# Kernel optimization log

Hardware: AMD Instinct MI355X
Metric: run time of the kernel (lower is better)

## Reference

```python
import jax, jax.numpy as jnp
import numpy as np

B, S, P, J = 32, 128, 2, 17
DIN, DOUT, DRNN, DHID = 2, 3, 128, 256
N = P * J
DT = 0.1   # delta_t from init
K = 4      # Euler steps, hardcoded k=int(4) in source


def setup_inputs() -> dict:
    key = jax.random.key(0)
    ks = jax.random.split(key, 12)
    g = lambda k, sh, fan: (jax.random.normal(k, sh, jnp.float32) / np.sqrt(fan)).astype(jnp.float32)
    d = {}
    d['x2d'] = jax.random.normal(ks[0], (B, S, P, J, DIN), jnp.float32)
    d['mask'] = jax.random.randint(ks[1], (B, S, P, J, 1), 0, 2).astype(jnp.int32)
    # ODE MLP: DRNN -> DHID -> DHID -> DRNN (num_hidden=2 hidden layers, tanh)
    d['ode_w0'] = g(ks[2], (DRNN, DHID), DRNN); d['ode_b0'] = jnp.zeros((DHID,), jnp.float32)
    d['ode_w1'] = g(ks[3], (DHID, DHID), DHID); d['ode_b1'] = jnp.zeros((DHID,), jnp.float32)
    d['ode_w2'] = g(ks[4], (DHID, DRNN), DHID); d['ode_b2'] = jnp.zeros((DRNN,), jnp.float32)
    # GRU cell 0: input DIN -> hidden DRNN ; GRU cell 1: input DRNN -> hidden DRNN
    d['wih0'] = g(ks[5], (DIN, 3 * DRNN), DIN);  d['whh0'] = g(ks[6], (DRNN, 3 * DRNN), DRNN)
    d['bih0'] = jnp.zeros((3 * DRNN,), jnp.float32); d['bhh0'] = jnp.zeros((3 * DRNN,), jnp.float32)
    d['wih1'] = g(ks[7], (DRNN, 3 * DRNN), DRNN); d['whh1'] = g(ks[8], (DRNN, 3 * DRNN), DRNN)
    d['bih1'] = jnp.zeros((3 * DRNN,), jnp.float32); d['bhh1'] = jnp.zeros((3 * DRNN,), jnp.float32)
    d['wout'] = g(ks[9], (DRNN, DOUT), DRNN); d['bout'] = jnp.zeros((DOUT,), jnp.float32)
    d['h0'] = 0.01 * jax.random.normal(ks[10], (1, 1, DRNN), jnp.float32)
    return d


def _ode(h, w0, b0, w1, b1, w2, b2):
    h = jnp.tanh(h @ w0 + b0)
    h = jnp.tanh(h @ w1 + b1)
    return h @ w2 + b2


def _gru(x, h, wih, whh, bih, bhh):
    gi = x @ wih + bih
    gh = h @ whh + bhh
    ir, iz, ig = jnp.split(gi, 3, axis=-1)
    hr, hz, hg = jnp.split(gh, 3, axis=-1)
    r = jax.nn.sigmoid(ir + hr)
    z = jax.nn.sigmoid(iz + hz)
    n = jnp.tanh(ig + r * hg)
    return (1.0 - z) * n + z * h


def reference(x2d, mask, ode_w0, ode_b0, ode_w1, ode_b1, ode_w2, ode_b2,
              wih0, whh0, bih0, bhh0, wih1, whh1, bih1, bhh1, wout, bout, h0):
    m = mask.astype(x2d.dtype)                      # (B,S,P,J,1)
    xs = (x2d * m).reshape(B, S, N, DIN)            # masked 2D input
    ms = m.reshape(B, S, N, 1)
    h_init = jnp.broadcast_to(h0, (B, N, DRNN))

    def step(h, inp):
        x, mm = inp                                 # (B,N,DIN), (B,N,1)
        h1 = h
        for _ in range(K):                          # 4 Euler ODE steps
            h1 = h1 + DT * _ode(h1, ode_w0, ode_b0, ode_w1, ode_b1, ode_w2, ode_b2)
        h2 = _gru(x, h1, wih0, whh0, bih0, bhh0)    # stacked GRU, both conditioned on h1
        h2 = _gru(h2, h1, wih1, whh1, bih1, bhh1)
        h_next = h1 * (1.0 - mm) + h2 * mm
        return h_next, h1

    _, hs = jax.lax.scan(step, h_init,
                         (jnp.swapaxes(xs, 0, 1), jnp.swapaxes(ms, 0, 1)))
    hs = jnp.swapaxes(hs, 0, 1)                     # (B,S,N,DRNN)
    ys = (hs @ wout + bout).reshape(B, S, P, J, DOUT)
    return ys
```

## Files before the change

kernel.cpp:

```cpp
#include <hip/hip_runtime.h>

typedef _Float16 f16x8 __attribute__((ext_vector_type(8)));
typedef float f32x4 __attribute__((ext_vector_type(4)));

constexpr int S_ = 128;
constexpr float DT_ = 0.1f;
constexpr float LS = 2048.0f;
constexpr float INV = 1.0f / 2048.0f;

#define MFMA(a, b, c) __builtin_amdgcn_mfma_f32_16x16x32_f16((a), (b), (c), 0, 0, 0)

#define OB0   0
#define OB1   256
#define OB2   512
#define OBHH0 640
#define OBIH0 1024
#define OBIH1 1408
#define OBHH1 1792
#define NBIAS 2176

__device__ __forceinline__ float fast_tanh(float x) {
    float e = __expf(2.0f * x);
    return 1.0f - 2.0f / (e + 1.0f);
}
__device__ __forceinline__ float fast_sigmoid(float x) {
    return 1.0f / (1.0f + __expf(-x));
}

template<int KT>
__device__ __forceinline__ void wtile_mm(
    const float* __restrict__ W, int N, int nt,
    const _Float16* __restrict__ Ah, const _Float16* __restrict__ Al, int lda,
    int lrow, int lk8, f32x4& acc, f32x4& pe, f32x4& qe)
{
    const float* base = W + (size_t)lk8 * N + nt * 16 + lrow;
    float raw[KT][8];
#pragma unroll
    for (int kt = 0; kt < KT; ++kt)
#pragma unroll
        for (int j = 0; j < 8; ++j)
            raw[kt][j] = base[(kt * 32 + j) * (size_t)N];
#pragma unroll
    for (int kt = 0; kt < KT; ++kt) {
        f16x8 bh, bl;
#pragma unroll
        for (int j = 0; j < 8; ++j) {
            float v = raw[kt][j];
            _Float16 h = (_Float16)v;
            bh[j] = h;
            bl[j] = (_Float16)((v - (float)h) * LS);
        }
        f16x8 ah = *(const f16x8*)(Ah + lrow * lda + kt * 32 + lk8);
        f16x8 al = *(const f16x8*)(Al + lrow * lda + kt * 32 + lk8);
        acc = MFMA(ah, bh, acc);
        pe  = MFMA(ah, bl, pe);
        qe  = MFMA(al, bh, qe);
    }
}

__global__ __launch_bounds__(512, 2) void odernn_mfma(
    const float* __restrict__ x2d, const int* __restrict__ maskp,
    const float* __restrict__ w0, const float* __restrict__ b0,
    const float* __restrict__ w1, const float* __restrict__ b1,
    const float* __restrict__ w2, const float* __restrict__ b2,
    const float* __restrict__ wih0, const float* __restrict__ whh0,
    const float* __restrict__ bih0, const float* __restrict__ bhh0,
    const float* __restrict__ wih1, const float* __restrict__ whh1,
    const float* __restrict__ bih1, const float* __restrict__ bhh1,
    const float* __restrict__ wout, const float* __restrict__ bout,
    const float* __restrict__ h0, float* __restrict__ out)
{
    __shared__ float hF[16][128];
    __shared__ _Float16 bAh[16][264], bAl[16][264];
    __shared__ _Float16 bBh[16][264], bBl[16][264];
    __shared__ _Float16 bHh[16][136], bHl[16][136];
    __shared__ float sbias[NBIAS];
    __shared__ float swi0[768];
    __shared__ float swout[384];
    __shared__ float sbout[4];
    __shared__ float sx0[16], sx1[16], smm[16];
    __shared__ int sIdx[16];

    const int tid = (int)threadIdx.x;
    const int wv = tid >> 6;
    const int l = tid & 63;
    const int lrow = l & 15;
    const int lk8 = (l >> 4) << 3;
    const int rbase = (l >> 4) << 2;

    for (int e = tid; e < 256; e += 512) { sbias[OB0 + e] = b0[e]; sbias[OB1 + e] = b1[e]; }
    for (int e = tid; e < 128; e += 512) sbias[OB2 + e] = b2[e];
    for (int e = tid; e < 384; e += 512) {
        sbias[OBHH0 + e] = bhh0[e];
        sbias[OBIH0 + e] = bih0[e];
        sbias[OBIH1 + e] = bih1[e];
        sbias[OBHH1 + e] = bhh1[e];
        swout[e] = wout[e];
    }
    for (int e = tid; e < 768; e += 512) swi0[e] = wih0[e];
    if (tid < 3) sbout[tid] = bout[tid];
    for (int e = tid; e < 2048; e += 512) {
        int row = e >> 7, col = e & 127;
        float v = h0[col];
        hF[row][col] = v;
        _Float16 hh = (_Float16)v;
        bHh[row][col] = hh;
        bHl[row][col] = (_Float16)((v - (float)hh) * LS);
    }
    if (tid < 16) {
        int grow = (int)blockIdx.x * 16 + tid;
        int bb = grow / 34, nn = grow - bb * 34;
        sIdx[tid] = bb * (S_ * 34) + nn;
    }
    __syncthreads();

    for (int s = 0; s < S_; ++s) {
        if (tid < 16) {
            int idx = sIdx[tid] + s * 34;
            float fm = (float)maskp[idx];
            smm[tid] = fm;
            sx0[tid] = x2d[2 * idx] * fm;
            sx1[tid] = x2d[2 * idx + 1] * fm;
        }

        for (int it = 0; it < 4; ++it) {
            {
                const int n0 = wv << 4, n1 = (wv + 8) << 4;
                float bv0 = sbias[OB0 + n0 + lrow], bv1 = sbias[OB0 + n1 + lrow];
                f32x4 a0 = {bv0, bv0, bv0, bv0}, a1 = {bv1, bv1, bv1, bv1};
                f32x4 p0 = {0, 0, 0, 0}, q0 = {0, 0, 0, 0}, p1 = {0, 0, 0, 0}, q1 = {0, 0, 0, 0};
                wtile_mm<4>(w0, 256, wv,     &bHh[0][0], &bHl[0][0], 136, lrow, lk8, a0, p0, q0);
                wtile_mm<4>(w0, 256, wv + 8, &bHh[0][0], &bHl[0][0], 136, lrow, lk8, a1, p1, q1);
#pragma unroll
                for (int r = 0; r < 4; ++r) {
                    int row = rbase + r;
                    float v0 = fast_tanh(a0[r] + (p0[r] + q0[r]) * INV);
                    float v1 = fast_tanh(a1[r] + (p1[r] + q1[r]) * INV);
                    _Float16 hh = (_Float16)v0;
                    bBh[row][n0 + lrow] = hh;
                    bBl[row][n0 + lrow] = (_Float16)((v0 - (float)hh) * LS);
                    hh = (_Float16)v1;
                    bBh[row][n1 + lrow] = hh;
                    bBl[row][n1 + lrow] = (_Float16)((v1 - (float)hh) * LS);
                }
            }
            __syncthreads();

            {
                const int n0 = wv << 4, n1 = (wv + 8) << 4;
                float bv0 = sbias[OB1 + n0 + lrow], bv1 = sbias[OB1 + n1 + lrow];
                f32x4 a0 = {bv0, bv0, bv0, bv0}, a1 = {bv1, bv1, bv1, bv1};
                f32x4 p0 = {0, 0, 0, 0}, q0 = {0, 0, 0, 0}, p1 = {0, 0, 0, 0}, q1 = {0, 0, 0, 0};
                wtile_mm<8>(w1, 256, wv,     &bBh[0][0], &bBl[0][0], 264, lrow, lk8, a0, p0, q0);
                wtile_mm<8>(w1, 256, wv + 8, &bBh[0][0], &bBl[0][0], 264, lrow, lk8, a1, p1, q1);
#pragma unroll
                for (int r = 0; r < 4; ++r) {
                    int row = rbase + r;
                    float v0 = fast_tanh(a0[r] + (p0[r] + q0[r]) * INV);
                    float v1 = fast_tanh(a1[r] + (p1[r] + q1[r]) * INV);
                    _Float16 hh = (_Float16)v0;
                    bAh[row][n0 + lrow] = hh;
                    bAl[row][n0 + lrow] = (_Float16)((v0 - (float)hh) * LS);
                    hh = (_Float16)v1;
                    bAh[row][n1 + lrow] = hh;
                    bAl[row][n1 + lrow] = (_Float16)((v1 - (float)hh) * LS);
                }
            }
            __syncthreads();

            {
                const int n0 = wv << 4;
                float bv = sbias[OB2 + n0 + lrow];
                f32x4 acc = {bv, bv, bv, bv};
                f32x4 pp = {0, 0, 0, 0}, qq = {0, 0, 0, 0};
                wtile_mm<8>(w2, 128, wv, &bAh[0][0], &bAl[0][0], 264, lrow, lk8, acc, pp, qq);
#pragma unroll
                for (int r = 0; r < 4; ++r) {
                    int row = rbase + r, col = n0 + lrow;
                    float v = hF[row][col] + DT_ * (acc[r] + (pp[r] + qq[r]) * INV);
                    hF[row][col] = v;
                    _Float16 hh = (_Float16)v;
                    bHh[row][col] = hh;
                    bHl[row][col] = (_Float16)((v - (float)hh) * LS);
                }
            }
            __syncthreads();
        }

        {
            f32x4 acc0, acc1, acc2;
            f32x4 p0 = {0,0,0,0}, q0 = {0,0,0,0}, p1 = {0,0,0,0}, q1 = {0,0,0,0}, p2 = {0,0,0,0}, q2 = {0,0,0,0};
            {
                float v0 = sbias[OBHH0 + ((wv) << 4) + lrow];
                float v1 = sbias[OBHH0 + ((wv + 8) << 4) + lrow];
                float v2 = sbias[OBHH0 + ((wv + 16) << 4) + lrow];
                acc0 = (f32x4){v0, v0, v0, v0};
                acc1 = (f32x4){v1, v1, v1, v1};
                acc2 = (f32x4){v2, v2, v2, v2};
            }
            wtile_mm<4>(whh0, 384, wv,      &bHh[0][0], &bHl[0][0], 136, lrow, lk8, acc0, p0, q0);
            wtile_mm<4>(whh0, 384, wv + 8,  &bHh[0][0], &bHl[0][0], 136, lrow, lk8, acc1, p1, q1);
            wtile_mm<4>(whh0, 384, wv + 16, &bHh[0][0], &bHl[0][0], 136, lrow, lk8, acc2, p2, q2);
            {
                int yrow = wv + ((l >> 5) << 3);
                int ll = l & 31;
                int c0 = ll << 2;
                float4 hv = *(const float4*)&hF[yrow][c0];
                float y0 = hv.x * swout[c0 * 3] + hv.y * swout[(c0 + 1) * 3] +
                           hv.z * swout[(c0 + 2) * 3] + hv.w * swout[(c0 + 3) * 3];
                float y1 = hv.x * swout[c0 * 3 + 1] + hv.y * swout[(c0 + 1) * 3 + 1] +
                           hv.z * swout[(c0 + 2) * 3 + 1] + hv.w * swout[(c0 + 3) * 3 + 1];
                float y2 = hv.x * swout[c0 * 3 + 2] + hv.y * swout[(c0 + 1) * 3 + 2] +
                           hv.z * swout[(c0 + 2) * 3 + 2] + hv.w * swout[(c0 + 3) * 3 + 2];
#pragma unroll
                for (int m = 16; m >= 1; m >>= 1) {
                    y0 += __shfl_xor(y0, m, 64);
                    y1 += __shfl_xor(y1, m, 64);
                    y2 += __shfl_xor(y2, m, 64);
                }
                if (ll == 0) {
                    int idx = sIdx[yrow] + s * 34;
                    out[idx * 3 + 0] = y0 + sbout[0];
                    out[idx * 3 + 1] = y1 + sbout[1];
                    out[idx * 3 + 2] = y2 + sbout[2];
                }
            }
            {
                int col = (wv << 4) + lrow;
                float wxr0 = swi0[col], wxr1 = swi0[384 + col];
                float wxz0 = swi0[128 + col], wxz1 = swi0[384 + 128 + col];
                float wxn0 = swi0[256 + col], wxn1 = swi0[384 + 256 + col];
                float bir = sbias[OBIH0 + col], biz = sbias[OBIH0 + 128 + col], bin = sbias[OBIH0 + 256 + col];
#pragma unroll
                for (int r = 0; r < 4; ++r) {
                    int row = rbase + r;
                    float ghr = acc0[r] + (p0[r] + q0[r]) * INV;
                    float ghz = acc1[r] + (p1[r] + q1[r]) * INV;
                    float ghn = acc2[r] + (p2[r] + q2[r]) * INV;
                    float xa = sx0[row], xb = sx1[row];
                    float rg = fast_sigmoid(bir + xa * wxr0 + xb * wxr1 + ghr);
                    float zg = fast_sigmoid(biz + xa * wxz0 + xb * wxz1 + ghz);
                    float nn = fast_tanh(bin + xa * wxn0 + xb * wxn1 + rg * ghn);
                    float h1 = hF[row][col];
                    float h2 = (1.0f - zg) * nn + zg * h1;
                    _Float16 hh = (_Float16)h2;
                    bBh[row][col] = hh;
                    bBl[row][col] = (_Float16)((h2 - (float)hh) * LS);
                }
            }
        }
        __syncthreads();

        {
            f32x4 gi0, gi1, gi2;
            {
                f32x4 a0, a1, a2;
                f32x4 p0 = {0,0,0,0}, q0 = {0,0,0,0}, p1 = {0,0,0,0}, q1 = {0,0,0,0}, p2 = {0,0,0,0}, q2 = {0,0,0,0};
                {
                    float v0 = sbias[OBIH1 + ((wv) << 4) + lrow];
                    float v1 = sbias[OBIH1 + ((wv + 8) << 4) + lrow];
                    float v2 = sbias[OBIH1 + ((wv + 16) << 4) + lrow];
                    a0 = (f32x4){v0, v0, v0, v0};
                    a1 = (f32x4){v1, v1, v1, v1};
                    a2 = (f32x4){v2, v2, v2, v2};
                }
                wtile_mm<4>(wih1, 384, wv,      &bBh[0][0], &bBl[0][0], 264, lrow, lk8, a0, p0, q0);
                wtile_mm<4>(wih1, 384, wv + 8,  &bBh[0][0], &bBl[0][0], 264, lrow, lk8, a1, p1, q1);
                wtile_mm<4>(wih1, 384, wv + 16, &bBh[0][0], &bBl[0][0], 264, lrow, lk8, a2, p2, q2);
                gi0 = a0 + (p0 + q0) * INV;
                gi1 = a1 + (p1 + q1) * INV;
                gi2 = a2 + (p2 + q2) * INV;
            }

            f32x4 aH0, aH1, aH2;
            f32x4 pH0 = {0,0,0,0}, qH0 = {0,0,0,0}, pH1 = {0,0,0,0}, qH1 = {0,0,0,0}, pH2 = {0,0,0,0}, qH2 = {0,0,0,0};
            {
                float v0 = sbias[OBHH1 + ((wv) << 4) + lrow];
                float v1 = sbias[OBHH1 + ((wv + 8) << 4) + lrow];
                float v2 = sbias[OBHH1 + ((wv + 16) << 4) + lrow];
                aH0 = (f32x4){v0, v0, v0, v0};
                aH1 = (f32x4){v1, v1, v1, v1};
                aH2 = (f32x4){v2, v2, v2, v2};
            }
            wtile_mm<4>(whh1, 384, wv,      &bHh[0][0], &bHl[0][0], 136, lrow, lk8, aH0, pH0, qH0);
            wtile_mm<4>(whh1, 384, wv + 8,  &bHh[0][0], &bHl[0][0], 136, lrow, lk8, aH1, pH1, qH1);
            wtile_mm<4>(whh1, 384, wv + 16, &bHh[0][0], &bHl[0][0], 136, lrow, lk8, aH2, pH2, qH2);

            __syncthreads();
#pragma unroll
            for (int r = 0; r < 4; ++r) {
                int row = rbase + r, col = (wv << 4) + lrow;
                float ghr = aH0[r] + (pH0[r] + qH0[r]) * INV;
                float ghz = aH1[r] + (pH1[r] + qH1[r]) * INV;
                float ghn = aH2[r] + (pH2[r] + qH2[r]) * INV;
                float rg = fast_sigmoid(gi0[r] + ghr);
                float zg = fast_sigmoid(gi1[r] + ghz);
                float nn = fast_tanh(gi2[r] + rg * ghn);
                float h1 = hF[row][col];
                float h2 = (1.0f - zg) * nn + zg * h1;
                float v = (smm[row] != 0.0f) ? h2 : h1;
                hF[row][col] = v;
                _Float16 hh = (_Float16)v;
                bHh[row][col] = hh;
                bHl[row][col] = (_Float16)((v - (float)hh) * LS);
            }
        }
        __syncthreads();
    }
}

extern "C" void kernel_launch(void* const* d_in, const int* in_sizes, int n_in,
                              void* d_out, int out_size, void* d_ws, size_t ws_size,
                              hipStream_t stream) {
    const float* x2d  = (const float*)d_in[0];
    const int*   mask = (const int*)d_in[1];
    const float* w0   = (const float*)d_in[2];
    const float* b0   = (const float*)d_in[3];
    const float* w1   = (const float*)d_in[4];
    const float* b1   = (const float*)d_in[5];
    const float* w2   = (const float*)d_in[6];
    const float* b2   = (const float*)d_in[7];
    const float* wih0 = (const float*)d_in[8];
    const float* whh0 = (const float*)d_in[9];
    const float* bih0 = (const float*)d_in[10];
    const float* bhh0 = (const float*)d_in[11];
    const float* wih1 = (const float*)d_in[12];
    const float* whh1 = (const float*)d_in[13];
    const float* bih1 = (const float*)d_in[14];
    const float* bhh1 = (const float*)d_in[15];
    const float* wout = (const float*)d_in[16];
    const float* bout = (const float*)d_in[17];
    const float* h0   = (const float*)d_in[18];
    float* out = (float*)d_out;

    hipLaunchKernelGGL(odernn_mfma, dim3(68), dim3(512), 0, stream,
        x2d, mask, w0, b0, w1, b1, w2, b2,
        wih0, whh0, bih0, bhh0, wih1, whh1, bih1, bhh1,
        wout, bout, h0, out);
}
```

Before: 7.217 ms.

## Pre-split weights into fp16 hi/lo tiles in MFMA fragment layout

Adds a prep kernel that converts each fp32 weight matrix once per call into fp16 high and scaled-low parts, stored in the exact per-lane MFMA B-fragment order in workspace. The main recurrent kernel then loads two contiguous 16-byte vectors per k-tile instead of eight strided fp32 loads plus conversion on every timestep. This removes repeated strided global gathers and conversion ALU work from the sequential loop. In exchange it adds six small prep launches and doubles weight storage in fp16 form. Launch bounds change from two blocks per CU to one, which relaxes register limits for the held fragments.

```diff
diff --git a/kernel.cpp b/kernel.cpp
--- a/kernel.cpp
+++ b/kernel.cpp
@@ -26,46 +26,61 @@
 __device__ __forceinline__ float fast_sigmoid(float x) {
     return 1.0f / (1.0f + __expf(-x));
 }
+__device__ __forceinline__ f32x4 bc4(float v) { return (f32x4){v, v, v, v}; }
+
+__global__ void prep_hl(const float* __restrict__ src, _Float16* __restrict__ hi,
+                        _Float16* __restrict__ lo, int K, int N) {
+    int e = blockIdx.x * 256 + threadIdx.x;
+    if (e >= K * N) return;
+    int tile = e >> 9, r = e & 511;
+    int lane = r >> 3, j = r & 7;
+    int KT = K >> 5;
+    int nt = tile / KT, kt = tile - nt * KT;
+    int k = kt * 32 + ((lane >> 4) << 3) + j;
+    int n = nt * 16 + (lane & 15);
+    float v = src[k * N + n];
+    _Float16 h = (_Float16)v;
+    hi[e] = h;
+    lo[e] = (_Float16)((v - (float)h) * LS);
+}
 
 template<int KT>
-__device__ __forceinline__ void wtile_mm(
-    const float* __restrict__ W, int N, int nt,
+__device__ __forceinline__ f32x4 tile_mm(
+    const _Float16* __restrict__ Wh, const _Float16* __restrict__ Wl, int nt,
     const _Float16* __restrict__ Ah, const _Float16* __restrict__ Al, int lda,
-    int lrow, int lk8, f32x4& acc, f32x4& pe, f32x4& qe)
+    int l, int lrow, int lk8, float bias)
 {
-    const float* base = W + (size_t)lk8 * N + nt * 16 + lrow;
-    float raw[KT][8];
-#pragma unroll
-    for (int kt = 0; kt < KT; ++kt)
-#pragma unroll
-        for (int j = 0; j < 8; ++j)
-            raw[kt][j] = base[(kt * 32 + j) * (size_t)N];
+    const _Float16* ph = Wh + ((size_t)nt * KT) * 512 + l * 8;
+    const _Float16* pl = Wl + ((size_t)nt * KT) * 512 + l * 8;
+    f16x8 bh[KT], bl[KT];
 #pragma unroll
     for (int kt = 0; kt < KT; ++kt) {
-        f16x8 bh, bl;
-#pragma unroll
-        for (int j = 0; j < 8; ++j) {
-            float v = raw[kt][j];
-            _Float16 h = (_Float16)v;
-            bh[j] = h;
-            bl[j] = (_Float16)((v - (float)h) * LS);
-        }
+        bh[kt] = *(const f16x8*)(ph + kt * 512);
+        bl[kt] = *(const f16x8*)(pl + kt * 512);
+    }
+    f32x4 acc = bc4(bias), pe = bc4(0.f), qe = bc4(0.f);
+#pragma unroll
+    for (int kt = 0; kt < KT; ++kt) {
         f16x8 ah = *(const f16x8*)(Ah + lrow * lda + kt * 32 + lk8);
         f16x8 al = *(const f16x8*)(Al + lrow * lda + kt * 32 + lk8);
-        acc = MFMA(ah, bh, acc);
-        pe  = MFMA(ah, bl, pe);
-        qe  = MFMA(al, bh, qe);
-    }
-}
-
-__global__ __launch_bounds__(512, 2) void odernn_mfma(
+        acc = MFMA(ah, bh[kt], acc);
+        pe  = MFMA(ah, bl[kt], pe);
+        qe  = MFMA(al, bh[kt], qe);
+    }
+    return acc + (pe + qe) * INV;
+}
+
+__global__ __launch_bounds__(512, 1) void odernn_mfma(
     const float* __restrict__ x2d, const int* __restrict__ maskp,
-    const float* __restrict__ w0, const float* __restrict__ b0,
-    const float* __restrict__ w1, const float* __restrict__ b1,
-    const float* __restrict__ w2, const float* __restrict__ b2,
-    const float* __restrict__ wih0, const float* __restrict__ whh0,
-    const float* __restrict__ bih0, const float* __restrict__ bhh0,
-    const float* __restrict__ wih1, const float* __restrict__ whh1,
+    const _Float16* __restrict__ w0h, const _Float16* __restrict__ w0l,
+    const _Float16* __restrict__ w1hg, const _Float16* __restrict__ w1lg,
+    const _Float16* __restrict__ w2h, const _Float16* __restrict__ w2l,
+    const _Float16* __restrict__ hh0h, const _Float16* __restrict__ hh0l,
+    const _Float16* __restrict__ ih1h, const _Float16* __restrict__ ih1l,
+    const _Float16* __restrict__ hh1h, const _Float16* __restrict__ hh1l,
+    const float* __restrict__ b0, const float* __restrict__ b1,
+    const float* __restrict__ b2, const float* __restrict__ bhh0,
+    const float* __restrict__ bih0, const float* __restrict__ wih0,
     const float* __restrict__ bih1, const float* __restrict__ bhh1,
     const float* __restrict__ wout, const float* __restrict__ bout,
     const float* __restrict__ h0, float* __restrict__ out)
@@ -125,59 +140,54 @@
 
         for (int it = 0; it < 4; ++it) {
             {
+                f32x4 v0 = tile_mm<4>(w0h, w0l, wv, &bHh[0][0], &bHl[0][0], 136,
+                                      l, lrow, lk8, sbias[OB0 + (wv << 4) + lrow]);
+                f32x4 v1 = tile_mm<4>(w0h, w0l, wv + 8, &bHh[0][0], &bHl[0][0], 136,
+                                      l, lrow, lk8, sbias[OB0 + ((wv + 8) << 4) + lrow]);
                 const int n0 = wv << 4, n1 = (wv + 8) << 4;
-                float bv0 = sbias[OB0 + n0 + lrow], bv1 = sbias[OB0 + n1 + lrow];
-                f32x4 a0 = {bv0, bv0, bv0, bv0}, a1 = {bv1, bv1, bv1, bv1};
-                f32x4 p0 = {0, 0, 0, 0}, q0 = {0, 0, 0, 0}, p1 = {0, 0, 0, 0}, q1 = {0, 0, 0, 0};
-                wtile_mm<4>(w0, 256, wv,     &bHh[0][0], &bHl[0][0], 136, lrow, lk8, a0, p0, q0);
-                wtile_mm<4>(w0, 256, wv + 8, &bHh[0][0], &bHl[0][0], 136, lrow, lk8, a1, p1, q1);
 #pragma unroll
                 for (int r = 0; r < 4; ++r) {
                     int row = rbase + r;
-                    float v0 = fast_tanh(a0[r] + (p0[r] + q0[r]) * INV);
-                    float v1 = fast_tanh(a1[r] + (p1[r] + q1[r]) * INV);
-                    _Float16 hh = (_Float16)v0;
+                    float t0 = fast_tanh(v0[r]);
+                    float t1 = fast_tanh(v1[r]);
+                    _Float16 hh = (_Float16)t0;
                     bBh[row][n0 + lrow] = hh;
-                    bBl[row][n0 + lrow] = (_Float16)((v0 - (float)hh) * LS);
-                    hh = (_Float16)v1;
+                    bBl[row][n0 + lrow] = (_Float16)((t0 - (float)hh) * LS);
+                    hh = (_Float16)t1;
                     bBh[row][n1 + lrow] = hh;
-                    bBl[row][n1 + lrow] = (_Float16)((v1 - (float)hh) * LS);
+                    bBl[row][n1 + lrow] = (_Float16)((t1 - (float)hh) * LS);
                 }
             }
             __syncthreads();
 
             {
+                f32x4 v0 = tile_mm<8>(w1hg, w1lg, wv, &bBh[0][0], &bBl[0][0], 264,
+                                      l, lrow, lk8, sbias[OB1 + (wv << 4) + lrow]);
+                f32x4 v1 = tile_mm<8>(w1hg, w1lg, wv + 8, &bBh[0][0], &bBl[0][0], 264,
+                                      l, lrow, lk8, sbias[OB1 + ((wv + 8) << 4) + lrow]);
                 const int n0 = wv << 4, n1 = (wv + 8) << 4;
-                float bv0 = sbias[OB1 + n0 + lrow], bv1 = sbias[OB1 + n1 + lrow];
-                f32x4 a0 = {bv0, bv0, bv0, bv0}, a1 = {bv1, bv1, bv1, bv1};
-                f32x4 p0 = {0, 0, 0, 0}, q0 = {0, 0, 0, 0}, p1 = {0, 0, 0, 0}, q1 = {0, 0, 0, 0};
-                wtile_mm<8>(w1, 256, wv,     &bBh[0][0], &bBl[0][0], 264, lrow, lk8, a0, p0, q0);
-                wtile_mm<8>(w1, 256, wv + 8, &bBh[0][0], &bBl[0][0], 264, lrow, lk8, a1, p1, q1);
 #pragma unroll
                 for (int r = 0; r < 4; ++r) {
                     int row = rbase + r;
-                    float v0 = fast_tanh(a0[r] + (p0[r] + q0[r]) * INV);
-                    float v1 = fast_tanh(a1[r] + (p1[r] + q1[r]) * INV);
-                    _Float16 hh = (_Float16)v0;
+                    float t0 = fast_tanh(v0[r]);
+                    float t1 = fast_tanh(v1[r]);
+                    _Float16 hh = (_Float16)t0;
                     bAh[row][n0 + lrow] = hh;
-                    bAl[row][n0 + lrow] = (_Float16)((v0 - (float)hh) * LS);
-                    hh = (_Float16)v1;
+                    bAl[row][n0 + lrow] = (_Float16)((t0 - (float)hh) * LS);
+                    hh = (_Float16)t1;
                     bAh[row][n1 + lrow] = hh;
-                    bAl[row][n1 + lrow] = (_Float16)((v1 - (float)hh) * LS);
+                    bAl[row][n1 + lrow] = (_Float16)((t1 - (float)hh) * LS);
                 }
             }
             __syncthreads();
 
             {
-                const int n0 = wv << 4;
-                float bv = sbias[OB2 + n0 + lrow];
-                f32x4 acc = {bv, bv, bv, bv};
-                f32x4 pp = {0, 0, 0, 0}, qq = {0, 0, 0, 0};
-                wtile_mm<8>(w2, 128, wv, &bAh[0][0], &bAl[0][0], 264, lrow, lk8, acc, pp, qq);
+                f32x4 f = tile_mm<8>(w2h, w2l, wv, &bAh[0][0], &bAl[0][0], 264,
+                                     l, lrow, lk8, sbias[OB2 + (wv << 4) + lrow]);
 #pragma unroll
                 for (int r = 0; r < 4; ++r) {
-                    int row = rbase + r, col = n0 + lrow;
-                    float v = hF[row][col] + DT_ * (acc[r] + (pp[r] + qq[r]) * INV);
+                    int row = rbase + r, col = (wv << 4) + lrow;
+                    float v = hF[row][col] + DT_ * f[r];
                     hF[row][col] = v;
                     _Float16 hh = (_Float16)v;
                     bHh[row][col] = hh;
@@ -188,19 +198,11 @@
         }
 
         {
-            f32x4 acc0, acc1, acc2;
-            f32x4 p0 = {0,0,0,0}, q0 = {0,0,0,0}, p1 = {0,0,0,0}, q1 = {0,0,0,0}, p2 = {0,0,0,0}, q2 = {0,0,0,0};
-            {
-                float v0 = sbias[OBHH0 + ((wv) << 4) + lrow];
-                float v1 = sbias[OBHH0 + ((wv + 8) << 4) + lrow];
-                float v2 = sbias[OBHH0 + ((wv + 16) << 4) + lrow];
-                acc0 = (f32x4){v0, v0, v0, v0};
-                acc1 = (f32x4){v1, v1, v1, v1};
-                acc2 = (f32x4){v2, v2, v2, v2};
-            }
-            wtile_mm<4>(whh0, 384, wv,      &bHh[0][0], &bHl[0][0], 136, lrow, lk8, acc0, p0, q0);
-            wtile_mm<4>(whh0, 384, wv + 8,  &bHh[0][0], &bHl[0][0], 136, lrow, lk8, acc1, p1, q1);
-            wtile_mm<4>(whh0, 384, wv + 16, &bHh[0][0], &bHl[0][0], 136, lrow, lk8, acc2, p2, q2);
+            f32x4 gh[3];
+#pragma unroll
+            for (int t = 0; t < 3; ++t)
+                gh[t] = tile_mm<4>(hh0h, hh0l, wv + (t << 3), &bHh[0][0], &bHl[0][0], 136,
+                                   l, lrow, lk8, sbias[OBHH0 + ((wv + (t << 3)) << 4) + lrow]);
             {
                 int yrow = wv + ((l >> 5) << 3);
                 int ll = l & 31;
@@ -234,13 +236,10 @@
 #pragma unroll
                 for (int r = 0; r < 4; ++r) {
                     int row = rbase + r;
-                    float ghr = acc0[r] + (p0[r] + q0[r]) * INV;
-                    float ghz = acc1[r] + (p1[r] + q1[r]) * INV;
-                    float ghn = acc2[r] + (p2[r] + q2[r]) * INV;
                     float xa = sx0[row], xb = sx1[row];
-                    float rg = fast_sigmoid(bir + xa * wxr0 + xb * wxr1 + ghr);
-                    float zg = fast_sigmoid(biz + xa * wxz0 + xb * wxz1 + ghz);
-                    float nn = fast_tanh(bin + xa * wxn0 + xb * wxn1 + rg * ghn);
+                    float rg = fast_sigmoid(bir + xa * wxr0 + xb * wxr1 + gh[0][r]);
+                    float zg = fast_sigmoid(biz + xa * wxz0 + xb * wxz1 + gh[1][r]);
+                    float nn = fast_tanh(bin + xa * wxn0 + xb * wxn1 + rg * gh[2][r]);
                     float h1 = hF[row][col];
                     float h2 = (1.0f - zg) * nn + zg * h1;
                     _Float16 hh = (_Float16)h2;
@@ -252,50 +251,23 @@
         __syncthreads();
 
         {
-            f32x4 gi0, gi1, gi2;
-            {
-                f32x4 a0, a1, a2;
-                f32x4 p0 = {0,0,0,0}, q0 = {0,0,0,0}, p1 = {0,0,0,0}, q1 = {0,0,0,0}, p2 = {0,0,0,0}, q2 = {0,0,0,0};
-                {
-                    float v0 = sbias[OBIH1 + ((wv) << 4) + lrow];
-                    float v1 = sbias[OBIH1 + ((wv + 8) << 4) + lrow];
-                    float v2 = sbias[OBIH1 + ((wv + 16) << 4) + lrow];
-                    a0 = (f32x4){v0, v0, v0, v0};
-                    a1 = (f32x4){v1, v1, v1, v1};
-                    a2 = (f32x4){v2, v2, v2, v2};
-                }
-                wtile_mm<4>(wih1, 384, wv,      &bBh[0][0], &bBl[0][0], 264, lrow, lk8, a0, p0, q0);
-                wtile_mm<4>(wih1, 384, wv + 8,  &bBh[0][0], &bBl[0][0], 264, lrow, lk8, a1, p1, q1);
-                wtile_mm<4>(wih1, 384, wv + 16, &bBh[0][0], &bBl[0][0], 264, lrow, lk8, a2, p2, q2);
-                gi0 = a0 + (p0 + q0) * INV;
-                gi1 = a1 + (p1 + q1) * INV;
-                gi2 = a2 + (p2 + q2) * INV;
-            }
-
-            f32x4 aH0, aH1, aH2;
-            f32x4 pH0 = {0,0,0,0}, qH0 = {0,0,0,0}, pH1 = {0,0,0,0}, qH1 = {0,0,0,0}, pH2 = {0,0,0,0}, qH2 = {0,0,0,0};
-            {
-                float v0 = sbias[OBHH1 + ((wv) << 4) + lrow];
-                float v1 = sbias[OBHH1 + ((wv + 8) << 4) + lrow];
-                float v2 = sbias[OBHH1 + ((wv + 16) << 4) + lrow];
-                aH0 = (f32x4){v0, v0, v0, v0};
-                aH1 = (f32x4){v1, v1, v1, v1};
-                aH2 = (f32x4){v2, v2, v2, v2};
-            }
-            wtile_mm<4>(whh1, 384, wv,      &bHh[0][0], &bHl[0][0], 136, lrow, lk8, aH0, pH0, qH0);
-            wtile_mm<4>(whh1, 384, wv + 8,  &bHh[0][0], &bHl[0][0], 136, lrow, lk8, aH1, pH1, qH1);
-            wtile_mm<4>(whh1, 384, wv + 16, &bHh[0][0], &bHl[0][0], 136, lrow, lk8, aH2, pH2, qH2);
+            f32x4 gi[3], gh[3];
+#pragma unroll
+            for (int t = 0; t < 3; ++t)
+                gi[t] = tile_mm<4>(ih1h, ih1l, wv + (t << 3), &bBh[0][0], &bBl[0][0], 264,
+                                   l, lrow, lk8, sbias[OBIH1 + ((wv + (t << 3)) << 4) + lrow]);
+#pragma unroll
+            for (int t = 0; t < 3; ++t)
+                gh[t] = tile_mm<4>(hh1h, hh1l, wv + (t << 3), &bHh[0][0], &bHl[0][0], 136,
+                                   l, lrow, lk8, sbias[OBHH1 + ((wv + (t << 3)) << 4) + lrow]);
 
             __syncthreads();
 #pragma unroll
             for (int r = 0; r < 4; ++r) {
                 int row = rbase + r, col = (wv << 4) + lrow;
-                float ghr = aH0[r] + (pH0[r] + qH0[r]) * INV;
-                float ghz = aH1[r] + (pH1[r] + qH1[r]) * INV;
-                float ghn = aH2[r] + (pH2[r] + qH2[r]) * INV;
-                float rg = fast_sigmoid(gi0[r] + ghr);
-                float zg = fast_sigmoid(gi1[r] + ghz);
-                float nn = fast_tanh(gi2[r] + rg * ghn);
+                float rg = fast_sigmoid(gi[0][r] + gh[0][r]);
+                float zg = fast_sigmoid(gi[1][r] + gh[1][r]);
+                float nn = fast_tanh(gi[2][r] + rg * gh[2][r]);
                 float h1 = hF[row][col];
                 float h2 = (1.0f - zg) * nn + zg * h1;
                 float v = (smm[row] != 0.0f) ? h2 : h1;
@@ -333,8 +305,30 @@
     const float* h0   = (const float*)d_in[18];
     float* out = (float*)d_out;
 
+    _Float16* base = (_Float16*)d_ws;
+    _Float16* pw0h  = base;
+    _Float16* pw1h  = base + 32768;
+    _Float16* pw2h  = base + 98304;
+    _Float16* ph0h  = base + 131072;
+    _Float16* pi1h  = base + 180224;
+    _Float16* ph1h  = base + 229376;
+    _Float16* lobase = base + 278528;
+    _Float16* pw0l  = lobase;
+    _Float16* pw1l  = lobase + 32768;
+    _Float16* pw2l  = lobase + 98304;
+    _Float16* ph0l  = lobase + 131072;
+    _Float16* pi1l  = lobase + 180224;
+    _Float16* ph1l  = lobase + 229376;
+
+    hipLaunchKernelGGL(prep_hl, dim3(128), dim3(256), 0, stream, w0,   pw0h, pw0l, 128, 256);
+    hipLaunchKernelGGL(prep_hl, dim3(256), dim3(256), 0, stream, w1,   pw1h, pw1l, 256, 256);
+    hipLaunchKernelGGL(prep_hl, dim3(128), dim3(256), 0, stream, w2,   pw2h, pw2l, 256, 128);
+    hipLaunchKernelGGL(prep_hl, dim3(192), dim3(256), 0, stream, whh0, ph0h, ph0l, 128, 384);
+    hipLaunchKernelGGL(prep_hl, dim3(192), dim3(256), 0, stream, wih1, pi1h, pi1l, 128, 384);
+    hipLaunchKernelGGL(prep_hl, dim3(192), dim3(256), 0, stream, whh1, ph1h, ph1l, 128, 384);
+
     hipLaunchKernelGGL(odernn_mfma, dim3(68), dim3(512), 0, stream,
-        x2d, mask, w0, b0, w1, b1, w2, b2,
-        wih0, whh0, bih0, bhh0, wih1, whh1, bih1, bhh1,
-        wout, bout, h0, out);
-}
+        x2d, mask, pw0h, pw0l, pw1h, pw1l, pw2h, pw2l,
+        ph0h, ph0l, pi1h, pi1l, ph1h, ph1l,
+        b0, b1, b2, bhh0, bih0, wih0, bih1, bhh1, wout, bout, h0, out);
+}
```

Result: faster. 6.895 ms (-4.5%).
